# Kernel optimization log

Hardware: AMD Instinct MI355X
Metric: run time of the kernel (lower is better)

Reference implementation:

```python
import jax, jax.numpy as jnp
import numpy as np

C = 1024      # channels
K = 7         # kernel_size
G = 1         # groups (G>1 crashes in the original torch code; see notes)
GC = C // G   # group_channels
OFFSET_SCALE = 2.0
LN_EPS = 1e-5


def setup_inputs() -> dict:
    key = jax.random.key(0)
    ks = jax.random.split(key, 8)
    N, L = 4, 2048
    s = 1.0 / np.sqrt(C)
    x = jax.random.normal(ks[0], (N, L, C), jnp.float32)
    Wi = jax.random.normal(ks[1], (C, C), jnp.float32) * s
    bi = jnp.zeros((C,), jnp.float32)
    dw_w = jax.random.normal(ks[2], (C, 1, 3), jnp.float32) * 0.5   # depthwise conv kernel (O, I/g=1, W)
    dw_b = jnp.zeros((C,), jnp.float32)
    ln_g = jnp.ones((C,), jnp.float32)
    ln_b = jnp.zeros((C,), jnp.float32)
    Wo = jax.random.normal(ks[3], (G * K, C), jnp.float32) * 0.02   # offset head (nonzero to exercise gather)
    bo = jnp.zeros((G * K,), jnp.float32)
    Wm = jax.random.normal(ks[4], (G * K, C), jnp.float32) * 0.02   # mask head
    bm = jnp.zeros((G * K,), jnp.float32)
    Wout = jax.random.normal(ks[5], (C, C), jnp.float32) * s
    bout = jnp.zeros((C,), jnp.float32)
    return {"x": x, "Wi": Wi, "bi": bi, "dw_w": dw_w, "dw_b": dw_b,
            "ln_g": ln_g, "ln_b": ln_b, "Wo": Wo, "bo": bo,
            "Wm": Wm, "bm": bm, "Wout": Wout, "bout": bout}


def _forward(x, Wi, bi, dw_w, dw_b, ln_g, ln_b, Wo, bo, Wm, bm, Wout, bout):
    N, L, Cc = x.shape
    dt = x.dtype
    # input projection
    x_proj = x @ Wi.T + bi                                  # [N,L,C]
    # depthwise conv (k=3, pad=1, groups=C) -> LayerNorm(C) -> GELU(exact)
    y = jax.lax.conv_general_dilated(
        x.transpose(0, 2, 1), dw_w, window_strides=(1,), padding=((1, 1),),
        dimension_numbers=("NCH", "OIH", "NCH"), feature_group_count=Cc)
    x_dw = y.transpose(0, 2, 1) + dw_b                       # [N,L,C]
    mu = x_dw.mean(-1, keepdims=True)
    var = ((x_dw - mu) ** 2).mean(-1, keepdims=True)
    x_dw = (x_dw - mu) * jax.lax.rsqrt(var + LN_EPS) * ln_g + ln_b
    x_dw = jax.nn.gelu(x_dw, approximate=False)
    # dynamic offsets and sampling mask
    offsets = (x_dw @ Wo.T + bo).reshape(N, L, G, K) * OFFSET_SCALE
    mask = jax.nn.softmax((x_dw @ Wm.T + bm).reshape(N, L, G, K), axis=-1)
    mask = jnp.nan_to_num(mask, nan=0.0)
    # absolute sampling positions
    ref_off = jnp.linspace(-(K // 2), K // 2, K).astype(dt)          # [K]
    pos = jnp.arange(L, dtype=dt)[None, :, None, None]               # [1,L,1,1]
    abs_pos = pos + ref_off[None, None, None, :] + offsets           # [N,L,G,K]
    apc = jnp.clip(abs_pos, 0.0, L - 1)
    p_floor = jnp.clip(apc.astype(jnp.int32), 0, L - 1)
    p_ceil = jnp.clip(p_floor + 1, 0, L - 1)
    w_ceil = apc - p_floor.astype(dt)
    w_floor = 1.0 - w_ceil
    valid = jnp.logical_not((abs_pos < 0) | (abs_pos > L - 1)).astype(dt)
    w_floor = w_floor * valid
    w_ceil = w_ceil * valid
    # gather + bilinear blend (G=1: each sample index grabs the full C channels)
    idx_f = p_floor.reshape(N, -1)[:, :, None]                       # [N, L*G*K, 1]
    idx_c = p_ceil.reshape(N, -1)[:, :, None]
    v_floor = jnp.take_along_axis(x_proj, idx_f, axis=1).reshape(N, L, G, K, GC)
    v_ceil = jnp.take_along_axis(x_proj, idx_c, axis=1).reshape(N, L, G, K, GC)
    sampled = v_floor * w_floor[..., None] + v_ceil * w_ceil[..., None]
    out = (sampled * mask[..., None]).sum(axis=3).reshape(N, L, Cc)  # sum over K
    return out @ Wout.T + bout


def reference(x, Wi, bi, dw_w, dw_b, ln_g, ln_b, Wo, bo, Wm, bm, Wout, bout):
    return _forward(x, Wi, bi, dw_w, dw_b, ln_g, ln_b, Wo, bo, Wm, bm, Wout, bout)
```

## Files before the change

kernel.cpp:

```cpp
#include <hip/hip_runtime.h>
#include <hip/hip_bf16.h>
#include <cstdint>

#define C_DIM 1024
#define L_DIM 2048
#define N_DIM 4
#define M_DIM (N_DIM * L_DIM)

typedef __attribute__((ext_vector_type(8))) short frag8;
typedef __attribute__((ext_vector_type(4)))  float f32x4;
typedef __attribute__((ext_vector_type(16))) float f32x16;

__device__ __forceinline__ void gl_lds16(const void* g, void* l) {
  __builtin_amdgcn_global_load_lds((const __attribute__((address_space(1))) void*)g,
                                   (__attribute__((address_space(3))) void*)l,
                                   16, 0, 0);
}
__device__ __forceinline__ void store_out(float* Y, size_t idx, float v) { Y[idx] = v; }
__device__ __forceinline__ void store_out(__hip_bfloat16* Y, size_t idx, float v) {
  Y[idx] = __float2bfloat16(v);
}
__device__ __forceinline__ float4 ldbf4(const __hip_bfloat16* p) {
  union { short4 s; __hip_bfloat16 h[4]; } u; u.s = *(const short4*)p;
  return make_float4((float)u.h[0], (float)u.h[1], (float)u.h[2], (float)u.h[3]);
}
__device__ __forceinline__ void stbf4(__hip_bfloat16* p, float4 v) {
  union { short4 s; __hip_bfloat16 h[4]; } u;
  u.h[0] = __float2bfloat16(v.x); u.h[1] = __float2bfloat16(v.y);
  u.h[2] = __float2bfloat16(v.z); u.h[3] = __float2bfloat16(v.w);
  *(short4*)p = u.s;
}
__device__ __forceinline__ float gelu_fast(float t) {
  const float t3 = t * t * t;
  const float ns = -1.5957691216f * t - 0.0713548163f * t3;
  return t / (1.f + __expf(ns));
}

__global__ __launch_bounds__(256)
void cvt_f32_bf16(const float* __restrict__ in, __hip_bfloat16* __restrict__ out, int n8) {
  const int i = blockIdx.x * 256 + threadIdx.x;
  if (i >= n8) return;
  const float4 a = *(const float4*)(in + (size_t)i * 8);
  const float4 b = *(const float4*)(in + (size_t)i * 8 + 4);
  union { __hip_bfloat16 h[8]; int4 q; } u;
  u.h[0] = __float2bfloat16(a.x); u.h[1] = __float2bfloat16(a.y);
  u.h[2] = __float2bfloat16(a.z); u.h[3] = __float2bfloat16(a.w);
  u.h[4] = __float2bfloat16(b.x); u.h[5] = __float2bfloat16(b.y);
  u.h[6] = __float2bfloat16(b.z); u.h[7] = __float2bfloat16(b.w);
  *(int4*)(out + (size_t)i * 8) = u.q;
}

template <typename TY>
__global__ __launch_bounds__(256, 2)
void gemm_db(const __hip_bfloat16* __restrict__ X,
             const __hip_bfloat16* __restrict__ W,
             const float* __restrict__ bias,
             TY* __restrict__ Y, int M, int N, int K)
{
  __shared__ __hip_bfloat16 As[2][2][128 * 32];
  __shared__ __hip_bfloat16 Bs[2][2][128 * 32];
  const int tid  = threadIdx.x;
  const int lane = tid & 63;
  const int wave = tid >> 6;
  const int bm = blockIdx.x * 128;
  const int bn = blockIdx.y * 128;
  const int wr = (wave >> 1) * 64;
  const int wc = (wave & 1) * 64;
  const int srow  = tid >> 2;
  const int skoff = (tid & 3) * 8;

  const __hip_bfloat16* gA0 = X + (size_t)(bm + srow) * K + skoff;
  const __hip_bfloat16* gA1 = X + (size_t)(bm + 64 + srow) * K + skoff;
  const __hip_bfloat16* gB0 = W + (size_t)(bn + srow) * K + skoff;
  const __hip_bfloat16* gB1 = W + (size_t)(bn + 64 + srow) * K + skoff;

  f32x16 acc[2][2] = {};
  const int arow  = lane & 31;
  const int akoff = (lane >> 5) * 8;

#define STAGE(k0, buf)                                        \
  do {                                                        \
    gl_lds16(gA0 + (k0),      &As[buf][0][tid * 8]);          \
    gl_lds16(gA1 + (k0),      &As[buf][0][2048 + tid * 8]);   \
    gl_lds16(gA0 + (k0) + 32, &As[buf][1][tid * 8]);          \
    gl_lds16(gA1 + (k0) + 32, &As[buf][1][2048 + tid * 8]);   \
    gl_lds16(gB0 + (k0),      &Bs[buf][0][tid * 8]);          \
    gl_lds16(gB1 + (k0),      &Bs[buf][0][2048 + tid * 8]);   \
    gl_lds16(gB0 + (k0) + 32, &Bs[buf][1][tid * 8]);          \
    gl_lds16(gB1 + (k0) + 32, &Bs[buf][1][2048 + tid * 8]);   \
  } while (0)

  STAGE(0, 0);
  __syncthreads();
  const int iters = K / 64;
  for (int it = 0; it < iters; ++it) {
    const int cur = it & 1;
    if (it + 1 < iters) STAGE((it + 1) * 64, cur ^ 1);

#pragma unroll
    for (int p = 0; p < 2; ++p)
#pragma unroll
      for (int h = 0; h < 2; ++h) {
        const frag8 a0 = *(const frag8*)&As[cur][p][(wr + arow) * 32 + h * 16 + akoff];
        const frag8 a1 = *(const frag8*)&As[cur][p][(wr + 32 + arow) * 32 + h * 16 + akoff];
        const frag8 b0 = *(const frag8*)&Bs[cur][p][(wc + arow) * 32 + h * 16 + akoff];
        const frag8 b1 = *(const frag8*)&Bs[cur][p][(wc + 32 + arow) * 32 + h * 16 + akoff];
        acc[0][0] = __builtin_amdgcn_mfma_f32_32x32x16_bf16(a0, b0, acc[0][0], 0, 0, 0);
        acc[0][1] = __builtin_amdgcn_mfma_f32_32x32x16_bf16(a0, b1, acc[0][1], 0, 0, 0);
        acc[1][0] = __builtin_amdgcn_mfma_f32_32x32x16_bf16(a1, b0, acc[1][0], 0, 0, 0);
        acc[1][1] = __builtin_amdgcn_mfma_f32_32x32x16_bf16(a1, b1, acc[1][1], 0, 0, 0);
      }
    __syncthreads();
  }
#undef STAGE

#pragma unroll
  for (int i = 0; i < 2; i++)
#pragma unroll
    for (int j = 0; j < 2; j++) {
      const int col = bn + wc + j * 32 + (lane & 31);
      const float bv = bias[col];
#pragma unroll
      for (int r = 0; r < 16; r++) {
        const int row = bm + wr + i * 32 + (r & 3) + 8 * (r >> 2) + 4 * (lane >> 5);
        store_out(Y, (size_t)row * N + col, acc[i][j][r] + bv);
      }
    }
}

struct Ld8f { float4 a, b; };
struct Ld8b { int4 a; };
__device__ __forceinline__ Ld8f ld8(const float* p) {
  return { *(const float4*)p, *(const float4*)(p + 4) };
}
__device__ __forceinline__ Ld8b ld8(const __hip_bfloat16* p) { return { *(const int4*)p }; }
__device__ __forceinline__ void st8(__hip_bfloat16* l, const Ld8f& v) {
  union { __hip_bfloat16 h[8]; int4 q; } u;
  u.h[0] = __float2bfloat16(v.a.x); u.h[1] = __float2bfloat16(v.a.y);
  u.h[2] = __float2bfloat16(v.a.z); u.h[3] = __float2bfloat16(v.a.w);
  u.h[4] = __float2bfloat16(v.b.x); u.h[5] = __float2bfloat16(v.b.y);
  u.h[6] = __float2bfloat16(v.b.z); u.h[7] = __float2bfloat16(v.b.w);
  *(int4*)l = u.q;
}
__device__ __forceinline__ void st8(__hip_bfloat16* l, const Ld8b& v) { *(int4*)l = v.a; }

template <typename TX, typename TY>
__global__ __launch_bounds__(256, 2)
void gemm_nt(const TX* __restrict__ X, const float* __restrict__ W,
             const float* __restrict__ bias, TY* __restrict__ Y, int M, int N, int K)
{
  __shared__ __hip_bfloat16 As[128 * 32];
  __shared__ __hip_bfloat16 Bs[128 * 32];
  const int tid  = threadIdx.x;
  const int lane = tid & 63;
  const int wave = tid >> 6;
  const int bm = blockIdx.x * 128;
  const int bn = blockIdx.y * 128;
  const int wr = (wave >> 1) * 64;
  const int wc = (wave & 1) * 64;
  const int srow  = tid >> 2;
  const int skoff = (tid & 3) * 8;

  f32x4 acc[4][4] = {};
  const TX*    gA0 = X + (size_t)(bm + srow) * K + skoff;
  const TX*    gA1 = X + (size_t)(bm + 64 + srow) * K + skoff;
  const float* gB0 = W + (size_t)(bn + srow) * K + skoff;
  const float* gB1 = W + (size_t)(bn + 64 + srow) * K + skoff;
  const int arow  = lane & 15;
  const int akoff = (lane >> 4) * 8;

  for (int k0 = 0; k0 < K; k0 += 32) {
    const auto va0 = ld8(gA0 + k0);
    const auto va1 = ld8(gA1 + k0);
    const auto vb0 = ld8(gB0 + k0);
    const auto vb1 = ld8(gB1 + k0);
    __syncthreads();
    st8(&As[srow * 32 + skoff],        va0);
    st8(&As[(64 + srow) * 32 + skoff], va1);
    st8(&Bs[srow * 32 + skoff],        vb0);
    st8(&Bs[(64 + srow) * 32 + skoff], vb1);
    __syncthreads();

    frag8 a[4], b[4];
#pragma unroll
    for (int i = 0; i < 4; i++)
      a[i] = *(const frag8*)&As[(wr + i * 16 + arow) * 32 + akoff];
#pragma unroll
    for (int j = 0; j < 4; j++)
      b[j] = *(const frag8*)&Bs[(wc + j * 16 + arow) * 32 + akoff];
#pragma unroll
    for (int i = 0; i < 4; i++)
#pragma unroll
      for (int j = 0; j < 4; j++)
        acc[i][j] = __builtin_amdgcn_mfma_f32_16x16x32_bf16(a[i], b[j], acc[i][j], 0, 0, 0);
  }
#pragma unroll
  for (int i = 0; i < 4; i++)
#pragma unroll
    for (int j = 0; j < 4; j++) {
      const int col = bn + wc + j * 16 + (lane & 15);
      const float bv = bias[col];
#pragma unroll
      for (int r = 0; r < 4; r++) {
        const int row = bm + wr + i * 16 + (lane >> 4) * 4 + r;
        store_out(Y, (size_t)row * N + col, acc[i][j][r] + bv);
      }
    }
}

__global__ __launch_bounds__(256)
void pre_fused(const float* __restrict__ x,
               const float* __restrict__ dw_w, const float* __restrict__ dw_b,
               const float* __restrict__ ln_g, const float* __restrict__ ln_b,
               const float* __restrict__ Wo,   const float* __restrict__ bo,
               const float* __restrict__ Wm,   const float* __restrict__ bmb,
               __hip_bfloat16* __restrict__ xbb,
               float* __restrict__ coef)
{
  const int b    = blockIdx.x;
  const int bs   = (b & 7) * 256 + (b >> 3);
  const int wid  = threadIdx.x >> 6;
  const int lane = threadIdx.x & 63;
  const int row  = bs * 4 + wid;
  const int l    = row & (L_DIM - 1);

  const float* xr = x + (size_t)row * C_DIM;
  __hip_bfloat16* xbr = xbb + (size_t)row * C_DIM;

  float4 v[4];
#pragma unroll
  for (int j = 0; j < 4; j++) {
    const int c4 = j * 256 + lane * 4;
    const float4 x0 = *(const float4*)(xr + c4);
    stbf4(xbr + c4, x0);
    float4 xm = make_float4(0.f, 0.f, 0.f, 0.f);
    float4 xq = make_float4(0.f, 0.f, 0.f, 0.f);
    if (l > 0)         xm = *(const float4*)(xr + c4 - C_DIM);
    if (l < L_DIM - 1) xq = *(const float4*)(xr + c4 + C_DIM);
    const float4 w0 = *(const float4*)(dw_w + (size_t)c4 * 3);
    const float4 w1 = *(const float4*)(dw_w + (size_t)c4 * 3 + 4);
    const float4 w2 = *(const float4*)(dw_w + (size_t)c4 * 3 + 8);
    const float4 bb = *(const float4*)(dw_b + c4);
    v[j].x = xm.x * w0.x + x0.x * w0.y + xq.x * w0.z + bb.x;
    v[j].y = xm.y * w0.w + x0.y * w1.x + xq.y * w1.y + bb.y;
    v[j].z = xm.z * w1.z + x0.z * w1.w + xq.z * w2.x + bb.z;
    v[j].w = xm.w * w2.y + x0.w * w2.z + xq.w * w2.w + bb.w;
  }

  float s1 = 0.f, s2 = 0.f;
#pragma unroll
  for (int j = 0; j < 4; j++) {
    s1 += v[j].x + v[j].y + v[j].z + v[j].w;
    s2 += v[j].x * v[j].x + v[j].y * v[j].y + v[j].z * v[j].z + v[j].w * v[j].w;
  }
#pragma unroll
  for (int m = 1; m < 64; m <<= 1) { s1 += __shfl_xor(s1, m); s2 += __shfl_xor(s2, m); }
  const float mu   = s1 * (1.f / C_DIM);
  const float rstd = rsqrtf(s2 * (1.f / C_DIM) - mu * mu + 1e-5f);

  float4 g[4];
#pragma unroll
  for (int j = 0; j < 4; j++) {
    const int c4 = j * 256 + lane * 4;
    const float4 gg = *(const float4*)(ln_g + c4);
    const float4 bb = *(const float4*)(ln_b + c4);
    g[j].x = gelu_fast((v[j].x - mu) * rstd * gg.x + bb.x);
    g[j].y = gelu_fast((v[j].y - mu) * rstd * gg.y + bb.y);
    g[j].z = gelu_fast((v[j].z - mu) * rstd * gg.z + bb.z);
    g[j].w = gelu_fast((v[j].w - mu) * rstd * gg.w + bb.w);
  }

  float po[7] = {0,0,0,0,0,0,0}, pm[7] = {0,0,0,0,0,0,0};
#pragma unroll
  for (int k = 0; k < 7; k++) {
#pragma unroll
    for (int j = 0; j < 4; j++) {
      const int c4 = j * 256 + lane * 4;
      const float4 wo = *(const float4*)(Wo + (size_t)k * C_DIM + c4);
      const float4 wm = *(const float4*)(Wm + (size_t)k * C_DIM + c4);
      po[k] += g[j].x * wo.x + g[j].y * wo.y + g[j].z * wo.z + g[j].w * wo.w;
      pm[k] += g[j].x * wm.x + g[j].y * wm.y + g[j].z * wm.z + g[j].w * wm.w;
    }
  }
#pragma unroll
  for (int k = 0; k < 7; k++)
#pragma unroll
    for (int m = 1; m < 64; m <<= 1) {
      po[k] += __shfl_xor(po[k], m);
      pm[k] += __shfl_xor(pm[k], m);
    }

  float lg[7], mx = -1e30f;
#pragma unroll
  for (int k = 0; k < 7; k++) { lg[k] = pm[k] + bmb[k]; mx = fmaxf(mx, lg[k]); }
  float se = 0.f, e[7];
#pragma unroll
  for (int k = 0; k < 7; k++) { e[k] = __expf(lg[k] - mx); se += e[k]; }
  const float inv = 1.f / se;

  if (lane == 0) {
    float pk[32];
#pragma unroll
    for (int k = 0; k < 7; k++) {
      const float msk = e[k] * inv;
      const float off = (po[k] + bo[k]) * 2.0f;
      const float ap  = (float)l + (float)(k - 3) + off;
      const float apc = fminf(fmaxf(ap, 0.f), (float)(L_DIM - 1));
      int f = (int)apc;
      int c = f + 1; if (c > L_DIM - 1) c = L_DIM - 1;
      const float w1  = apc - (float)f;
      const float val = (ap < 0.f || ap > (float)(L_DIM - 1)) ? 0.f : 1.f;
      pk[k]      = (1.f - w1) * val * msk;
      pk[8 + k]  = w1 * val * msk;
      pk[16 + k] = (float)f;
      pk[24 + k] = (float)c;
    }
    pk[7] = pk[15] = pk[23] = pk[31] = 0.f;
    float* cr = coef + (size_t)row * 32;
#pragma unroll
    for (int q = 0; q < 8; q++)
      *(float4*)(cr + q * 4) = make_float4(pk[q*4], pk[q*4+1], pk[q*4+2], pk[q*4+3]);
  }
}

__global__ __launch_bounds__(256)
void gather_k(const float* __restrict__ coef,
              const __hip_bfloat16* __restrict__ xp,
              __hip_bfloat16* __restrict__ smp)
{
  const int b    = blockIdx.x;
  const int bs   = (b & 7) * 256 + (b >> 3);
  const int wid  = threadIdx.x >> 6;
  const int lane = threadIdx.x & 63;
  const int row  = bs * 4 + wid;
  const int n    = row >> 11;

  const float* cr = coef + (size_t)row * 32;
  const float4 q0 = *(const float4*)(cr);
  const float4 q1 = *(const float4*)(cr + 4);
  const float4 q2 = *(const float4*)(cr + 8);
  const float4 q3 = *(const float4*)(cr + 12);
  const float4 q4 = *(const float4*)(cr + 16);
  const float4 q5 = *(const float4*)(cr + 20);
  const float4 q6 = *(const float4*)(cr + 24);
  const float4 q7 = *(const float4*)(cr + 28);

  const float wf[7] = {q0.x, q0.y, q0.z, q0.w, q1.x, q1.y, q1.z};
  const float wc[7] = {q2.x, q2.y, q2.z, q2.w, q3.x, q3.y, q3.z};
  const int   pf[7] = {(int)q4.x, (int)q4.y, (int)q4.z, (int)q4.w, (int)q5.x, (int)q5.y, (int)q5.z};
  const int   pc[7] = {(int)q6.x, (int)q6.y, (int)q6.z, (int)q6.w, (int)q7.x, (int)q7.y, (int)q7.z};

  const __hip_bfloat16* xpn = xp + ((size_t)n * L_DIM) * C_DIM;
  __hip_bfloat16* so = smp + (size_t)row * C_DIM;

#pragma unroll
  for (int j = 0; j < 2; j++) {
    const int c8 = j * 512 + lane * 8;
    float a[8] = {0.f, 0.f, 0.f, 0.f, 0.f, 0.f, 0.f, 0.f};
#pragma unroll
    for (int k = 0; k < 7; k++) {
      union { int4 q; __hip_bfloat16 h[8]; } uf, uc;
      uf.q = *(const int4*)(xpn + (size_t)pf[k] * C_DIM + c8);
      uc.q = *(const int4*)(xpn + (size_t)pc[k] * C_DIM + c8);
#pragma unroll
      for (int t = 0; t < 8; t++)
        a[t] += wf[k] * (float)uf.h[t] + wc[k] * (float)uc.h[t];
    }
    union { int4 q; __hip_bfloat16 h[8]; } uo;
#pragma unroll
    for (int t = 0; t < 8; t++) uo.h[t] = __float2bfloat16(a[t]);
    *(int4*)(so + c8) = uo.q;
  }
}

__global__ __launch_bounds__(256)
void mid_fused_v4(const float* __restrict__ x,
                  const float* __restrict__ dw_w, const float* __restrict__ dw_b,
                  const float* __restrict__ ln_g, const float* __restrict__ ln_b,
                  const float* __restrict__ Wo,   const float* __restrict__ bo,
                  const float* __restrict__ Wm,   const float* __restrict__ bmb,
                  const __hip_bfloat16* __restrict__ xp,
                  __hip_bfloat16* __restrict__ smp)
{
  const int b    = blockIdx.x;
  const int bs   = (b & 7) * 256 + (b >> 3);
  const int wid  = threadIdx.x >> 6;
  const int lane = threadIdx.x & 63;
  const int row  = bs * 4 + wid;
  const int l    = row & (L_DIM - 1);
  const int n    = row >> 11;

  const float* xr = x + (size_t)row * C_DIM;

  float4 v[4];
#pragma unroll
  for (int j = 0; j < 4; j++) {
    const int c4 = j * 256 + lane * 4;
    const float4 x0 = *(const float4*)(xr + c4);
    float4 xm = make_float4(0.f, 0.f, 0.f, 0.f);
    float4 xq = make_float4(0.f, 0.f, 0.f, 0.f);
    if (l > 0)         xm = *(const float4*)(xr + c4 - C_DIM);
    if (l < L_DIM - 1) xq = *(const float4*)(xr + c4 + C_DIM);
    const float4 w0 = *(const float4*)(dw_w + (size_t)c4 * 3);
    const float4 w1 = *(const float4*)(dw_w + (size_t)c4 * 3 + 4);
    const float4 w2 = *(const float4*)(dw_w + (size_t)c4 * 3 + 8);
    const float4 bb = *(const float4*)(dw_b + c4);
    v[j].x = xm.x * w0.x + x0.x * w0.y + xq.x * w0.z + bb.x;
    v[j].y = xm.y * w0.w + x0.y * w1.x + xq.y * w1.y + bb.y;
    v[j].z = xm.z * w1.z + x0.z * w1.w + xq.z * w2.x + bb.z;
    v[j].w = xm.w * w2.y + x0.w * w2.z + xq.w * w2.w + bb.w;
  }

  float s1 = 0.f, s2 = 0.f;
#pragma unroll
  for (int j = 0; j < 4; j++) {
    s1 += v[j].x + v[j].y + v[j].z + v[j].w;
    s2 += v[j].x * v[j].x + v[j].y * v[j].y + v[j].z * v[j].z + v[j].w * v[j].w;
  }
#pragma unroll
  for (int m = 1; m < 64; m <<= 1) { s1 += __shfl_xor(s1, m); s2 += __shfl_xor(s2, m); }
  const float mu   = s1 * (1.f / C_DIM);
  const float rstd = rsqrtf(s2 * (1.f / C_DIM) - mu * mu + 1e-5f);

  float4 g[4];
#pragma unroll
  for (int j = 0; j < 4; j++) {
    const int c4 = j * 256 + lane * 4;
    const float4 gg = *(const float4*)(ln_g + c4);
    const float4 bb = *(const float4*)(ln_b + c4);
    g[j].x = gelu_fast((v[j].x - mu) * rstd * gg.x + bb.x);
    g[j].y = gelu_fast((v[j].y - mu) * rstd * gg.y + bb.y);
    g[j].z = gelu_fast((v[j].z - mu) * rstd * gg.z + bb.z);
    g[j].w = gelu_fast((v[j].w - mu) * rstd * gg.w + bb.w);
  }

  float po[7] = {0,0,0,0,0,0,0}, pm[7] = {0,0,0,0,0,0,0};
#pragma unroll
  for (int k = 0; k < 7; k++) {
#pragma unroll
    for (int j = 0; j < 4; j++) {
      const int c4 = j * 256 + lane * 4;
      const float4 wo = *(const float4*)(Wo + (size_t)k * C_DIM + c4);
      const float4 wm = *(const float4*)(Wm + (size_t)k * C_DIM + c4);
      po[k] += g[j].x * wo.x + g[j].y * wo.y + g[j].z * wo.z + g[j].w * wo.w;
      pm[k] += g[j].x * wm.x + g[j].y * wm.y + g[j].z * wm.z + g[j].w * wm.w;
    }
  }
#pragma unroll
  for (int k = 0; k < 7; k++)
#pragma unroll
    for (int m = 1; m < 64; m <<= 1) {
      po[k] += __shfl_xor(po[k], m);
      pm[k] += __shfl_xor(pm[k], m);
    }

  float lg[7], mx = -1e30f;
#pragma unroll
  for (int k = 0; k < 7; k++) { lg[k] = pm[k] + bmb[k]; mx = fmaxf(mx, lg[k]); }
  float se = 0.f, e[7];
#pragma unroll
  for (int k = 0; k < 7; k++) { e[k] = __expf(lg[k] - mx); se += e[k]; }
  const float inv = 1.f / se;

  float wf[7], wcl[7]; int pf[7], pc[7];
#pragma unroll
  for (int k = 0; k < 7; k++) {
    const float msk = e[k] * inv;
    const float off = (po[k] + bo[k]) * 2.0f;
    const float ap  = (float)l + (float)(k - 3) + off;
    const float apc = fminf(fmaxf(ap, 0.f), (float)(L_DIM - 1));
    int f = (int)apc;
    int c = f + 1; if (c > L_DIM - 1) c = L_DIM - 1;
    const float w1  = apc - (float)f;
    const float val = (ap < 0.f || ap > (float)(L_DIM - 1)) ? 0.f : 1.f;
    wf[k]  = (1.f - w1) * val * msk;
    wcl[k] = w1 * val * msk;
    pf[k] = f; pc[k] = c;
  }

  const __hip_bfloat16* xpn = xp + ((size_t)n * L_DIM) * C_DIM;
  __hip_bfloat16* so = smp + (size_t)row * C_DIM;
#pragma unroll
  for (int j = 0; j < 4; j++) {
    const int c4 = j * 256 + lane * 4;
    float4 a = make_float4(0.f, 0.f, 0.f, 0.f);
#pragma unroll
    for (int k = 0; k < 7; k++) {
      const float4 vf = ldbf4(xpn + (size_t)pf[k] * C_DIM + c4);
      const float4 vc = ldbf4(xpn + (size_t)pc[k] * C_DIM + c4);
      a.x += wf[k] * vf.x + wcl[k] * vc.x;
      a.y += wf[k] * vf.y + wcl[k] * vc.y;
      a.z += wf[k] * vf.z + wcl[k] * vc.z;
      a.w += wf[k] * vf.w + wcl[k] * vc.w;
    }
    stbf4(so + c4, a);
  }
}

extern "C" void kernel_launch(void* const* d_in, const int* in_sizes, int n_in,
                              void* d_out, int out_size, void* d_ws, size_t ws_size,
                              hipStream_t stream)
{
  const float* x    = (const float*)d_in[0];
  const float* Wi   = (const float*)d_in[1];
  const float* bi   = (const float*)d_in[2];
  const float* dw_w = (const float*)d_in[3];
  const float* dw_b = (const float*)d_in[4];
  const float* ln_g = (const float*)d_in[5];
  const float* ln_b = (const float*)d_in[6];
  const float* Wo   = (const float*)d_in[7];
  const float* bo   = (const float*)d_in[8];
  const float* Wm   = (const float*)d_in[9];
  const float* bm   = (const float*)d_in[10];
  const float* Wout = (const float*)d_in[11];
  const float* bout = (const float*)d_in[12];
  float* out = (float*)d_out;

  const size_t XE = (size_t)M_DIM * C_DIM;
  const size_t WE = (size_t)C_DIM * C_DIM;
  char* wsb = (char*)d_ws;
  __hip_bfloat16* xp    = (__hip_bfloat16*)wsb;
  __hip_bfloat16* smp   = (__hip_bfloat16*)(wsb + XE * 2);
  __hip_bfloat16* Wib   = (__hip_bfloat16*)(wsb + XE * 4);
  __hip_bfloat16* Woutb = (__hip_bfloat16*)(wsb + XE * 4 + WE * 2);
  __hip_bfloat16* xbb   = (__hip_bfloat16*)(wsb + XE * 4 + WE * 4);
  float*          coef  = (float*)(wsb + XE * 4 + WE * 4 + XE * 2);

  const size_t need_w2    = XE * 4 + WE * 4;
  const size_t need_full  = need_w2 + XE * 2;
  const size_t need_full2 = need_full + (size_t)M_DIM * 32 * 4;

  dim3 gg(M_DIM / 128, C_DIM / 128);

  if (ws_size >= need_full2) {
    cvt_f32_bf16<<<(int)(WE / 8 / 256), 256, 0, stream>>>(Wi, Wib, (int)(WE / 8));
    cvt_f32_bf16<<<(int)(WE / 8 / 256), 256, 0, stream>>>(Wout, Woutb, (int)(WE / 8));
    pre_fused<<<M_DIM / 4, 256, 0, stream>>>(x, dw_w, dw_b, ln_g, ln_b, Wo, bo, Wm, bm, xbb, coef);
    gemm_db<__hip_bfloat16><<<gg, 256, 0, stream>>>(xbb, Wib, bi, xp, M_DIM, C_DIM, C_DIM);
    gather_k<<<M_DIM / 4, 256, 0, stream>>>(coef, xp, smp);
    gemm_db<float><<<gg, 256, 0, stream>>>(smp, Woutb, bout, out, M_DIM, C_DIM, C_DIM);
  } else if (ws_size >= need_full) {
    cvt_f32_bf16<<<(int)(XE / 8 / 256), 256, 0, stream>>>(x, xbb, (int)(XE / 8));
    cvt_f32_bf16<<<(int)(WE / 8 / 256), 256, 0, stream>>>(Wi, Wib, (int)(WE / 8));
    cvt_f32_bf16<<<(int)(WE / 8 / 256), 256, 0, stream>>>(Wout, Woutb, (int)(WE / 8));
    gemm_db<__hip_bfloat16><<<gg, 256, 0, stream>>>(xbb, Wib, bi, xp, M_DIM, C_DIM, C_DIM);
    mid_fused_v4<<<M_DIM / 4, 256, 0, stream>>>(x, dw_w, dw_b, ln_g, ln_b, Wo, bo, Wm, bm, xp, smp);
    gemm_db<float><<<gg, 256, 0, stream>>>(smp, Woutb, bout, out, M_DIM, C_DIM, C_DIM);
  } else if (ws_size >= need_w2) {
    cvt_f32_bf16<<<(int)(WE / 8 / 256), 256, 0, stream>>>(Wout, Woutb, (int)(WE / 8));
    gemm_nt<float, __hip_bfloat16><<<gg, 256, 0, stream>>>(x, Wi, bi, xp, M_DIM, C_DIM, C_DIM);
    mid_fused_v4<<<M_DIM / 4, 256, 0, stream>>>(x, dw_w, dw_b, ln_g, ln_b, Wo, bo, Wm, bm, xp, smp);
    gemm_db<float><<<gg, 256, 0, stream>>>(smp, Woutb, bout, out, M_DIM, C_DIM, C_DIM);
  } else {
    gemm_nt<float, __hip_bfloat16><<<gg, 256, 0, stream>>>(x, Wi, bi, xp, M_DIM, C_DIM, C_DIM);
    mid_fused_v4<<<M_DIM / 4, 256, 0, stream>>>(x, dw_w, dw_b, ln_g, ln_b, Wo, bo, Wm, bm, xp, smp);
    gemm_nt<__hip_bfloat16, float><<<gg, 256, 0, stream>>>(smp, Wout, bout, out, M_DIM, C_DIM, C_DIM);
  }
}
```

Baseline: 207.2 us.

## Process four rows per wave in pre-fused kernel with LDS-staged head weights

The pre-fused conv/LayerNorm/GELU/offset-head kernel now handles four consecutive rows per wave instead of one. Neighbouring x rows are loaded once and reused across the depthwise conv. The Wo/Wm head weights and LN params are staged once per block into LDS via global_load_lds and reused for 16 rows. Paired shuffle reductions cut the butterfly cost by folding two sums into one pass. The trade-off is higher register and LDS use (64KB), which lowers occupancy, plus a quarter as many blocks.

```diff
diff --git a/kernel.cpp b/kernel.cpp
--- a/kernel.cpp
+++ b/kernel.cpp
@@ -208,118 +208,170 @@
     }
 }
 
-__global__ __launch_bounds__(256)
-void pre_fused(const float* __restrict__ x,
-               const float* __restrict__ dw_w, const float* __restrict__ dw_b,
-               const float* __restrict__ ln_g, const float* __restrict__ ln_b,
-               const float* __restrict__ Wo,   const float* __restrict__ bo,
-               const float* __restrict__ Wm,   const float* __restrict__ bmb,
-               __hip_bfloat16* __restrict__ xbb,
-               float* __restrict__ coef)
+__global__ __launch_bounds__(256, 2)
+void pre_fused_v2(const float* __restrict__ x,
+                  const float* __restrict__ dw_w, const float* __restrict__ dw_b,
+                  const float* __restrict__ ln_g, const float* __restrict__ ln_b,
+                  const float* __restrict__ Wo,   const float* __restrict__ bo,
+                  const float* __restrict__ Wm,   const float* __restrict__ bmb,
+                  __hip_bfloat16* __restrict__ xbb,
+                  float* __restrict__ coef)
 {
+  __shared__ float sW[16384];
+  float* sWo  = sW;
+  float* sWm  = sW + 7168;
+  float* slng = sW + 14336;
+  float* slnb = sW + 15360;
+
+  const int tid  = threadIdx.x;
+  const int lane = tid & 63;
+  const int wid  = tid >> 6;
+
+#pragma unroll
+  for (int i = 0; i < 7; i++)
+    gl_lds16(Wo + (size_t)(i * 256 + tid) * 4, &sWo[(i * 256 + tid) * 4]);
+#pragma unroll
+  for (int i = 0; i < 7; i++)
+    gl_lds16(Wm + (size_t)(i * 256 + tid) * 4, &sWm[(i * 256 + tid) * 4]);
+  gl_lds16(ln_g + (size_t)tid * 4, &slng[tid * 4]);
+  gl_lds16(ln_b + (size_t)tid * 4, &slnb[tid * 4]);
+  __syncthreads();
+
   const int b    = blockIdx.x;
-  const int bs   = (b & 7) * 256 + (b >> 3);
-  const int wid  = threadIdx.x >> 6;
-  const int lane = threadIdx.x & 63;
-  const int row  = bs * 4 + wid;
-  const int l    = row & (L_DIM - 1);
-
-  const float* xr = x + (size_t)row * C_DIM;
-  __hip_bfloat16* xbr = xbb + (size_t)row * C_DIM;
-
-  float4 v[4];
+  const int bs   = (b & 7) * 64 + (b >> 3);
+  const int row0 = bs * 16 + wid * 4;
+  const int l0   = row0 & (L_DIM - 1);
+
+  const float* xr = x + (size_t)row0 * C_DIM;
+
+  float4 v[4][4];
 #pragma unroll
   for (int j = 0; j < 4; j++) {
     const int c4 = j * 256 + lane * 4;
-    const float4 x0 = *(const float4*)(xr + c4);
-    stbf4(xbr + c4, x0);
-    float4 xm = make_float4(0.f, 0.f, 0.f, 0.f);
-    float4 xq = make_float4(0.f, 0.f, 0.f, 0.f);
-    if (l > 0)         xm = *(const float4*)(xr + c4 - C_DIM);
-    if (l < L_DIM - 1) xq = *(const float4*)(xr + c4 + C_DIM);
+    float4 xv[6];
+#pragma unroll
+    for (int m = 0; m < 6; m++) {
+      const int lm = l0 + m - 1;
+      if (lm >= 0 && lm < L_DIM)
+        xv[m] = *(const float4*)(xr + ((long)m - 1) * C_DIM + c4);
+      else
+        xv[m] = make_float4(0.f, 0.f, 0.f, 0.f);
+    }
+#pragma unroll
+    for (int r = 0; r < 4; r++)
+      stbf4(xbb + (size_t)(row0 + r) * C_DIM + c4, xv[r + 1]);
+
     const float4 w0 = *(const float4*)(dw_w + (size_t)c4 * 3);
     const float4 w1 = *(const float4*)(dw_w + (size_t)c4 * 3 + 4);
     const float4 w2 = *(const float4*)(dw_w + (size_t)c4 * 3 + 8);
     const float4 bb = *(const float4*)(dw_b + c4);
-    v[j].x = xm.x * w0.x + x0.x * w0.y + xq.x * w0.z + bb.x;
-    v[j].y = xm.y * w0.w + x0.y * w1.x + xq.y * w1.y + bb.y;
-    v[j].z = xm.z * w1.z + x0.z * w1.w + xq.z * w2.x + bb.z;
-    v[j].w = xm.w * w2.y + x0.w * w2.z + xq.w * w2.w + bb.w;
-  }
-
-  float s1 = 0.f, s2 = 0.f;
-#pragma unroll
-  for (int j = 0; j < 4; j++) {
-    s1 += v[j].x + v[j].y + v[j].z + v[j].w;
-    s2 += v[j].x * v[j].x + v[j].y * v[j].y + v[j].z * v[j].z + v[j].w * v[j].w;
-  }
-#pragma unroll
-  for (int m = 1; m < 64; m <<= 1) { s1 += __shfl_xor(s1, m); s2 += __shfl_xor(s2, m); }
-  const float mu   = s1 * (1.f / C_DIM);
-  const float rstd = rsqrtf(s2 * (1.f / C_DIM) - mu * mu + 1e-5f);
-
-  float4 g[4];
+#pragma unroll
+    for (int r = 0; r < 4; r++) {
+      const float4 xm = xv[r], x0 = xv[r + 1], xq = xv[r + 2];
+      v[r][j].x = xm.x * w0.x + x0.x * w0.y + xq.x * w0.z + bb.x;
+      v[r][j].y = xm.y * w0.w + x0.y * w1.x + xq.y * w1.y + bb.y;
+      v[r][j].z = xm.z * w1.z + x0.z * w1.w + xq.z * w2.x + bb.z;
+      v[r][j].w = xm.w * w2.y + x0.w * w2.z + xq.w * w2.w + bb.w;
+    }
+  }
+
+  float mu[4], rstd[4];
+#pragma unroll
+  for (int r = 0; r < 4; r++) {
+    float s1 = 0.f, s2 = 0.f;
+#pragma unroll
+    for (int j = 0; j < 4; j++) {
+      s1 += v[r][j].x + v[r][j].y + v[r][j].z + v[r][j].w;
+      s2 += v[r][j].x * v[r][j].x + v[r][j].y * v[r][j].y
+          + v[r][j].z * v[r][j].z + v[r][j].w * v[r][j].w;
+    }
+    const float t1 = s1 + __shfl_xor(s1, 32);
+    const float t2 = s2 + __shfl_xor(s2, 32);
+    float cc = (lane < 32) ? t1 : t2;
+#pragma unroll
+    for (int m = 16; m >= 1; m >>= 1) cc += __shfl_xor(cc, m);
+    const float dd = __shfl_xor(cc, 32);
+    const float S1 = (lane < 32) ? cc : dd;
+    const float S2 = (lane < 32) ? dd : cc;
+    mu[r]   = S1 * (1.f / C_DIM);
+    rstd[r] = rsqrtf(S2 * (1.f / C_DIM) - mu[r] * mu[r] + 1e-5f);
+  }
+
+  float po[4][7] = {}, pm[4][7] = {};
 #pragma unroll
   for (int j = 0; j < 4; j++) {
     const int c4 = j * 256 + lane * 4;
-    const float4 gg = *(const float4*)(ln_g + c4);
-    const float4 bb = *(const float4*)(ln_b + c4);
-    g[j].x = gelu_fast((v[j].x - mu) * rstd * gg.x + bb.x);
-    g[j].y = gelu_fast((v[j].y - mu) * rstd * gg.y + bb.y);
-    g[j].z = gelu_fast((v[j].z - mu) * rstd * gg.z + bb.z);
-    g[j].w = gelu_fast((v[j].w - mu) * rstd * gg.w + bb.w);
-  }
-
-  float po[7] = {0,0,0,0,0,0,0}, pm[7] = {0,0,0,0,0,0,0};
-#pragma unroll
-  for (int k = 0; k < 7; k++) {
-#pragma unroll
-    for (int j = 0; j < 4; j++) {
-      const int c4 = j * 256 + lane * 4;
-      const float4 wo = *(const float4*)(Wo + (size_t)k * C_DIM + c4);
-      const float4 wm = *(const float4*)(Wm + (size_t)k * C_DIM + c4);
-      po[k] += g[j].x * wo.x + g[j].y * wo.y + g[j].z * wo.z + g[j].w * wo.w;
-      pm[k] += g[j].x * wm.x + g[j].y * wm.y + g[j].z * wm.z + g[j].w * wm.w;
-    }
-  }
-#pragma unroll
-  for (int k = 0; k < 7; k++)
-#pragma unroll
-    for (int m = 1; m < 64; m <<= 1) {
-      po[k] += __shfl_xor(po[k], m);
-      pm[k] += __shfl_xor(pm[k], m);
-    }
-
-  float lg[7], mx = -1e30f;
-#pragma unroll
-  for (int k = 0; k < 7; k++) { lg[k] = pm[k] + bmb[k]; mx = fmaxf(mx, lg[k]); }
-  float se = 0.f, e[7];
-#pragma unroll
-  for (int k = 0; k < 7; k++) { e[k] = __expf(lg[k] - mx); se += e[k]; }
-  const float inv = 1.f / se;
-
-  if (lane == 0) {
-    float pk[32];
+    const float4 gg = *(const float4*)&slng[c4];
+    const float4 bb = *(const float4*)&slnb[c4];
+    float4 g[4];
+#pragma unroll
+    for (int r = 0; r < 4; r++) {
+      g[r].x = gelu_fast((v[r][j].x - mu[r]) * rstd[r] * gg.x + bb.x);
+      g[r].y = gelu_fast((v[r][j].y - mu[r]) * rstd[r] * gg.y + bb.y);
+      g[r].z = gelu_fast((v[r][j].z - mu[r]) * rstd[r] * gg.z + bb.z);
+      g[r].w = gelu_fast((v[r][j].w - mu[r]) * rstd[r] * gg.w + bb.w);
+    }
 #pragma unroll
     for (int k = 0; k < 7; k++) {
-      const float msk = e[k] * inv;
-      const float off = (po[k] + bo[k]) * 2.0f;
-      const float ap  = (float)l + (float)(k - 3) + off;
-      const float apc = fminf(fmaxf(ap, 0.f), (float)(L_DIM - 1));
-      int f = (int)apc;
-      int c = f + 1; if (c > L_DIM - 1) c = L_DIM - 1;
-      const float w1  = apc - (float)f;
-      const float val = (ap < 0.f || ap > (float)(L_DIM - 1)) ? 0.f : 1.f;
-      pk[k]      = (1.f - w1) * val * msk;
-      pk[8 + k]  = w1 * val * msk;
-      pk[16 + k] = (float)f;
-      pk[24 + k] = (float)c;
-    }
-    pk[7] = pk[15] = pk[23] = pk[31] = 0.f;
-    float* cr = coef + (size_t)row * 32;
-#pragma unroll
-    for (int q = 0; q < 8; q++)
-      *(float4*)(cr + q * 4) = make_float4(pk[q*4], pk[q*4+1], pk[q*4+2], pk[q*4+3]);
+      const float4 wo = *(const float4*)&sWo[k * 1024 + c4];
+      const float4 wm = *(const float4*)&sWm[k * 1024 + c4];
+#pragma unroll
+      for (int r = 0; r < 4; r++) {
+        po[r][k] += g[r].x * wo.x + g[r].y * wo.y + g[r].z * wo.z + g[r].w * wo.w;
+        pm[r][k] += g[r].x * wm.x + g[r].y * wm.y + g[r].z * wm.z + g[r].w * wm.w;
+      }
+    }
+  }
+
+  float poS[4][7], pmS[4][7];
+#pragma unroll
+  for (int r = 0; r < 4; r++)
+#pragma unroll
+    for (int k = 0; k < 7; k++) {
+      const float tp = po[r][k] + __shfl_xor(po[r][k], 32);
+      const float tm = pm[r][k] + __shfl_xor(pm[r][k], 32);
+      float cc = (lane < 32) ? tp : tm;
+#pragma unroll
+      for (int m = 16; m >= 1; m >>= 1) cc += __shfl_xor(cc, m);
+      const float dd = __shfl_xor(cc, 32);
+      poS[r][k] = (lane < 32) ? cc : dd;
+      pmS[r][k] = (lane < 32) ? dd : cc;
+    }
+
+#pragma unroll
+  for (int r = 0; r < 4; r++) {
+    float lg[7], mx = -1e30f;
+#pragma unroll
+    for (int k = 0; k < 7; k++) { lg[k] = pmS[r][k] + bmb[k]; mx = fmaxf(mx, lg[k]); }
+    float se = 0.f, e[7];
+#pragma unroll
+    for (int k = 0; k < 7; k++) { e[k] = __expf(lg[k] - mx); se += e[k]; }
+    const float inv = 1.f / se;
+    const int l = l0 + r;
+
+    if (lane == r) {
+      float pk[32];
+#pragma unroll
+      for (int k = 0; k < 7; k++) {
+        const float msk = e[k] * inv;
+        const float off = (poS[r][k] + bo[k]) * 2.0f;
+        const float ap  = (float)l + (float)(k - 3) + off;
+        const float apc = fminf(fmaxf(ap, 0.f), (float)(L_DIM - 1));
+        int f = (int)apc;
+        int c = f + 1; if (c > L_DIM - 1) c = L_DIM - 1;
+        const float w1  = apc - (float)f;
+        const float val = (ap < 0.f || ap > (float)(L_DIM - 1)) ? 0.f : 1.f;
+        pk[k]      = (1.f - w1) * val * msk;
+        pk[8 + k]  = w1 * val * msk;
+        pk[16 + k] = (float)f;
+        pk[24 + k] = (float)c;
+      }
+      pk[7] = pk[15] = pk[23] = pk[31] = 0.f;
+      float* cr = coef + (size_t)(row0 + r) * 32;
+#pragma unroll
+      for (int q = 0; q < 8; q++)
+        *(float4*)(cr + q * 4) = make_float4(pk[q*4], pk[q*4+1], pk[q*4+2], pk[q*4+3]);
+    }
   }
 }
 
@@ -535,7 +587,7 @@
   if (ws_size >= need_full2) {
     cvt_f32_bf16<<<(int)(WE / 8 / 256), 256, 0, stream>>>(Wi, Wib, (int)(WE / 8));
     cvt_f32_bf16<<<(int)(WE / 8 / 256), 256, 0, stream>>>(Wout, Woutb, (int)(WE / 8));
-    pre_fused<<<M_DIM / 4, 256, 0, stream>>>(x, dw_w, dw_b, ln_g, ln_b, Wo, bo, Wm, bm, xbb, coef);
+    pre_fused_v2<<<M_DIM / 16, 256, 0, stream>>>(x, dw_w, dw_b, ln_g, ln_b, Wo, bo, Wm, bm, xbb, coef);
     gemm_db<__hip_bfloat16><<<gg, 256, 0, stream>>>(xbb, Wib, bi, xp, M_DIM, C_DIM, C_DIM);
     gather_k<<<M_DIM / 4, 256, 0, stream>>>(coef, xp, smp);
     gemm_db<float><<<gg, 256, 0, stream>>>(smp, Woutb, bout, out, M_DIM, C_DIM, C_DIM);
```

Result: faster. 199.5 us (-3.8%).
